# Kernel tuning notes

Measured on AMD Instinct MI355X. Metric: run time of the kernel, lower is better.

## Reference

```python
import jax, jax.numpy as jnp
import numpy as np

DIM = 128
SQRT_DIM = float(np.sqrt(DIM))


def setup_inputs() -> dict:
    key = jax.random.key(0)
    k1, k2, k3, k4 = jax.random.split(key, 4)
    B, S, D = 16, 2048, DIM
    return {
        "query": jax.random.normal(k1, (B, S, D), dtype=jnp.float32),
        "key": jax.random.normal(k2, (B, S, D), dtype=jnp.float32),
        "value": jax.random.normal(k3, (B, S, D), dtype=jnp.float32),
        "trust_score": jax.random.uniform(k4, (B, 1, S), dtype=jnp.float32, minval=0.05, maxval=1.0),
    }


def reference(query, key, value, trust_score):
    # score: [B, q, k]
    score = jnp.einsum("bqd,bkd->bqk", query, key) / SQRT_DIM
    score = score * trust_score
    attn = jax.nn.softmax(score, axis=-1)
    # trust reweighting + renormalization
    attn = attn * trust_score
    attn = attn / jnp.sum(attn, axis=-1, keepdims=True)
    context = jnp.einsum("bqk,bkd->bqd", attn, value)
    return context
```

## Files before the change

kernel.cpp:

```cpp
#include <hip/hip_runtime.h>
#include <math.h>

#define SEQ 2048
#define DIM 128
#define KVB 32
#define NTILES (SEQ / KVB)
#define NT2 (NTILES / 2)
#define KTB 8192
#define VTB 8192

typedef __attribute__((ext_vector_type(8))) short bf16x8;
typedef __attribute__((ext_vector_type(16))) float f32x16;
typedef __attribute__((ext_vector_type(4))) short short4v;
typedef __attribute__((ext_vector_type(4))) float f32x4;

union frag_u { bf16x8 h; unsigned u[4]; };

__device__ __forceinline__ short f2bf(float f) {
  union { float f; unsigned u; } v; v.f = f;
  unsigned r = v.u + 0x7FFFu + ((v.u >> 16) & 1u);
  return (short)(r >> 16);
}
__device__ __forceinline__ float bf2f(short h) {
  return __uint_as_float(((unsigned)(unsigned short)h) << 16);
}
__device__ __forceinline__ void dma16(const void* g, void* l) {
  __builtin_amdgcn_global_load_lds(
      (const __attribute__((address_space(1))) void*)g,
      (__attribute__((address_space(3))) void*)l, 16, 0, 0);
}
__device__ __forceinline__ unsigned cvtpk(float lo, float hi) {
  unsigned r;
  asm("v_cvt_pk_bf16_f32 %0, %1, %2" : "=v"(r) : "v"(lo), "v"(hi));
  return r;
}
__device__ __forceinline__ void pl32swap(unsigned& a, unsigned& b) {
  asm("v_permlane32_swap_b32 %0, %1" : "+v"(a), "+v"(b));
}

__global__ __launch_bounds__(256)
void prepack_kernel(const float* __restrict__ Kg, const float* __restrict__ Vg,
                    const float* __restrict__ Tg,
                    char* __restrict__ Kws, char* __restrict__ Vws,
                    unsigned* __restrict__ Lws) {
  const int tile = blockIdx.x, b = blockIdx.y;
  const int tid = (int)threadIdx.x;
  const float* Kb = Kg + ((size_t)b * SEQ + tile * KVB) * DIM;
  const float* Vb = Vg + ((size_t)b * SEQ + tile * KVB) * DIM;
  const float* Tb = Tg + (size_t)b * SEQ + tile * KVB;
  char* kd = Kws + (size_t)(b * NTILES + tile) * KTB;
  char* vd = Vws + (size_t)(b * NTILES + tile) * VTB;

  #pragma unroll
  for (int i = 0; i < 2; ++i) {
    int id = i * 256 + tid;
    int k = id >> 4, c16 = id & 15;
    float sc = Tb[k] * 0.12751743f;
    const float4 f0 = *(const float4*)(Kb + (size_t)k * DIM + c16 * 8);
    const float4 f1 = *(const float4*)(Kb + (size_t)k * DIM + c16 * 8 + 4);
    bf16x8 pk;
    pk[0]=f2bf(f0.x*sc); pk[1]=f2bf(f0.y*sc); pk[2]=f2bf(f0.z*sc); pk[3]=f2bf(f0.w*sc);
    pk[4]=f2bf(f1.x*sc); pk[5]=f2bf(f1.y*sc); pk[6]=f2bf(f1.z*sc); pk[7]=f2bf(f1.w*sc);
    *(bf16x8*)(kd + k * 256 + ((c16 ^ (k & 7)) << 4)) = pk;
  }
  #pragma unroll
  for (int i = 0; i < 2; ++i) {
    int id = i * 256 + tid;
    int d = id & 127, ch = id >> 7;
    const float* src = Vb + (size_t)(ch * 8) * DIM + d;
    bf16x8 pk;
    #pragma unroll
    for (int j = 0; j < 8; ++j) pk[j] = f2bf(src[(size_t)j * DIM]);
    *(bf16x8*)(vd + d * 64 + ((ch ^ ((d >> 1) & 3)) << 4)) = pk;
  }
  if (tid < KVB) {
    float t = Tb[tid];
    float lt = log2f(t);
    short h = f2bf(lt);
    short lo = f2bf(lt - bf2f(h));
    Lws[(size_t)b * SEQ + tile * KVB + tid] =
        (unsigned)(unsigned short)h | ((unsigned)(unsigned short)lo << 16);
  }
}

__global__ __launch_bounds__(256, 2)
void trust_attn_main(const float* __restrict__ Qg, const char* __restrict__ Kws,
                     const char* __restrict__ Vws, const unsigned* __restrict__ Lws,
                     float* __restrict__ Og, int swz) {
  __shared__ __align__(16) char smem[65536];

  const int bid = (int)blockIdx.x;
  int b, qblk;
  if (swz) { int xcd = bid & 7, idx = bid >> 3; b = xcd * 2 + (idx >> 5); qblk = idx & 31; }
  else     { b = bid >> 5; qblk = bid & 31; }

  const int tid = (int)threadIdx.x;
  const int h   = tid >> 7;
  const int gq  = (tid >> 6) & 1;
  const int l   = tid & 63;
  const int hi  = l >> 5, l31 = l & 31;
  const int t128 = tid & 127;
  const int qcol = qblk * 64 + gq * 32 + l31;

  const float* Qr = Qg + ((size_t)b * SEQ + qcol) * DIM;
  const char* Kt = Kws + (size_t)(b * NTILES + h * NT2) * KTB;
  const char* Vt = Vws + (size_t)(b * NTILES + h * NT2) * VTB;
  const unsigned* Lb = Lws + (size_t)b * SEQ + h * (NT2 * KVB);

  frag_u qf[8];
  #pragma unroll
  for (int c = 0; c < 8; ++c) {
    const float4 a = *(const float4*)(Qr + c * 16 + hi * 8);
    const float4 d = *(const float4*)(Qr + c * 16 + hi * 8 + 4);
    bf16x8 q8;
    q8[0]=f2bf(a.x); q8[1]=f2bf(a.y); q8[2]=f2bf(a.z); q8[3]=f2bf(a.w);
    q8[4]=f2bf(d.x); q8[5]=f2bf(d.y); q8[6]=f2bf(d.z); q8[7]=f2bf(d.w);
    qf[c].h = q8;
  }
  frag_u qpad;
  qpad.u[0] = (hi == 0) ? 0x3F803F80u : 0u;
  qpad.u[1] = qpad.u[2] = qpad.u[3] = 0u;

  f32x16 acc[4];
  #pragma unroll
  for (int nt = 0; nt < 4; ++nt)
    #pragma unroll
    for (int i = 0; i < 16; ++i) acc[nt][i] = 0.f;
  float lsum = 0.f;

  auto ISSUE = [&](int t, int buf) {
    const char* ks = Kt + (size_t)t * KTB;
    const char* vs = Vt + (size_t)t * VTB;
    char* kl = smem + (h * 2 + buf) * 8192;
    char* vl = smem + 32768 + (h * 2 + buf) * 8192;
    #pragma unroll
    for (int j = 0; j < 2; ++j) {
      dma16(ks + j * 4096 + t128 * 16, kl + j * 4096 + t128 * 16);
      dma16(ks + j * 4096 + 2048 + t128 * 16, kl + j * 4096 + 2048 + t128 * 16);
      dma16(vs + j * 4096 + t128 * 16, vl + j * 4096 + t128 * 16);
      dma16(vs + j * 4096 + 2048 + t128 * 16, vl + j * 4096 + 2048 + t128 * 16);
    }
  };

  ISSUE(0, 0);
  unsigned ltc = Lb[l31];
  __syncthreads();

  for (int t = 0; t < NT2; ++t) {
    const int cur = t & 1;
    unsigned ltn = 0;
    if (t + 1 < NT2) {
      ISSUE(t + 1, cur ^ 1);
      ltn = Lb[(t + 1) * KVB + l31];
    }

    const char* Kc = smem + (h * 2 + cur) * 8192;
    const char* Vc = smem + 32768 + (h * 2 + cur) * 8192;

    f32x16 S;
    #pragma unroll
    for (int i = 0; i < 16; ++i) S[i] = 0.f;
    #pragma unroll
    for (int c = 0; c < 8; ++c) {
      frag_u kf;
      kf.h = *(const bf16x8*)(Kc + l31 * 256 + (((2 * c + hi) ^ (l31 & 7)) << 4));
      S = __builtin_amdgcn_mfma_f32_32x32x16_bf16(kf.h, qf[c].h, S, 0, 0, 0);
    }
    frag_u pa;
    pa.u[0] = (hi == 0) ? ltc : 0u;
    pa.u[1] = pa.u[2] = pa.u[3] = 0u;
    S = __builtin_amdgcn_mfma_f32_32x32x16_bf16(pa.h, qpad.h, S, 0, 0, 0);

    float p[16];
    #pragma unroll
    for (int i = 0; i < 16; ++i) {
      p[i] = __builtin_amdgcn_exp2f(S[i]);
      lsum += p[i];
    }

    frag_u PA[2];
    #pragma unroll
    for (int ks = 0; ks < 2; ++ks) {
      unsigned a0 = cvtpk(p[8*ks+0], p[8*ks+1]);
      unsigned a1 = cvtpk(p[8*ks+2], p[8*ks+3]);
      unsigned b0 = cvtpk(p[8*ks+4], p[8*ks+5]);
      unsigned b1 = cvtpk(p[8*ks+6], p[8*ks+7]);
      pl32swap(a0, b0);
      pl32swap(a1, b1);
      PA[ks].u[0] = a0; PA[ks].u[1] = a1; PA[ks].u[2] = b0; PA[ks].u[3] = b1;
    }

    #pragma unroll
    for (int nt = 0; nt < 4; ++nt)
      #pragma unroll
      for (int ks = 0; ks < 2; ++ks) {
        frag_u vf;
        vf.h = *(const bf16x8*)(Vc + (nt * 32 + l31) * 64 + (((2 * ks + hi) ^ ((l31 >> 1) & 3)) << 4));
        acc[nt] = __builtin_amdgcn_mfma_f32_32x32x16_bf16(vf.h, PA[ks].h, acc[nt], 0, 0, 0);
      }

    ltc = ltn;
    __syncthreads();
  }

  const float Z = lsum + __shfl_xor(lsum, 32);
  float* AccX = (float*)smem;
  float* Zx   = (float*)(smem + 32768);
  const int q2 = gq * 32 + l31;

  if (h == 1) {
    if (hi == 0) Zx[q2] = Z;
    #pragma unroll
    for (int nt = 0; nt < 4; ++nt)
      #pragma unroll
      for (int j = 0; j < 4; ++j) {
        int d = nt * 32 + j * 8 + hi * 4;
        int byte_off = (q2 * 512 + d * 4) ^ ((l31 & 7) << 4);
        f32x4 qd;
        qd[0] = acc[nt][j*4+0]; qd[1] = acc[nt][j*4+1];
        qd[2] = acc[nt][j*4+2]; qd[3] = acc[nt][j*4+3];
        *(f32x4*)((char*)AccX + byte_off) = qd;
      }
  }
  __syncthreads();
  if (h == 0) {
    const float inv = 1.0f / (Z + Zx[q2]);
    float* orow = Og + ((size_t)b * SEQ + qcol) * DIM;
    #pragma unroll
    for (int nt = 0; nt < 4; ++nt)
      #pragma unroll
      for (int j = 0; j < 4; ++j) {
        int d = nt * 32 + j * 8 + hi * 4;
        int byte_off = (q2 * 512 + d * 4) ^ ((l31 & 7) << 4);
        f32x4 o = *(const f32x4*)((const char*)AccX + byte_off);
        float4 r;
        r.x = (acc[nt][j*4+0] + o[0]) * inv;
        r.y = (acc[nt][j*4+1] + o[1]) * inv;
        r.z = (acc[nt][j*4+2] + o[2]) * inv;
        r.w = (acc[nt][j*4+3] + o[3]) * inv;
        *(float4*)(orow + d) = r;
      }
  }
}

__global__ __launch_bounds__(256, 2)
void trust_attn_fallback(const float* __restrict__ Qg, const float* __restrict__ Kg,
                         const float* __restrict__ Vg, const float* __restrict__ Tg,
                         float* __restrict__ Og) {
  __shared__ short Klds[2][64 * DIM];
  __shared__ short Vlds[2][DIM * 64];
  __shared__ short Plds[4][16 * 64];
  __shared__ float Tlds[2][64];

  const int b = blockIdx.y;
  const int qbase = blockIdx.x * 64;
  const int tid = (int)threadIdx.x;
  const int w = tid >> 6;
  const int l = tid & 63;
  const int lr = l & 15;
  const int lg = l >> 4;

  const float* Qb = Qg + (size_t)b * SEQ * DIM;
  const float* Kb = Kg + (size_t)b * SEQ * DIM;
  const float* Vb = Vg + (size_t)b * SEQ * DIM;
  const float* Tb = Tg + (size_t)b * SEQ;
  float*       Ob = Og + (size_t)b * SEQ * DIM;

  float4 kreg[8];
  float  vreg[32];
  float  treg;

  auto ISSUE = [&](int kv0) {
    #pragma unroll
    for (int i = 0; i < 8; ++i) {
      int flat4 = i * 256 + tid;
      int r = flat4 >> 5;
      int c4 = (flat4 & 31) << 2;
      kreg[i] = *(const float4*)(Kb + (size_t)(kv0 + r) * DIM + c4);
    }
    #pragma unroll
    for (int i = 0; i < 4; ++i) {
      int task = i * 256 + tid;
      int d = task & 127;
      int chunk = task >> 7;
      const float* src = Vb + (size_t)(kv0 + chunk * 8) * DIM + d;
      #pragma unroll
      for (int j = 0; j < 8; ++j) vreg[i * 8 + j] = src[(size_t)j * DIM];
    }
    treg = (tid < 64) ? Tb[kv0 + tid] : 0.f;
  };

  auto STORE = [&](int buf) {
    #pragma unroll
    for (int i = 0; i < 8; ++i) {
      int flat4 = i * 256 + tid;
      int r = flat4 >> 5;
      int c4 = (flat4 & 31) << 2;
      short4v pk;
      pk[0] = f2bf(kreg[i].x); pk[1] = f2bf(kreg[i].y);
      pk[2] = f2bf(kreg[i].z); pk[3] = f2bf(kreg[i].w);
      int byte_off = (r * 256 + (c4 << 1)) ^ ((r & 7) << 4);
      *(short4v*)((char*)&Klds[buf][0] + byte_off) = pk;
    }
    #pragma unroll
    for (int i = 0; i < 4; ++i) {
      int task = i * 256 + tid;
      int d = task & 127;
      int chunk = task >> 7;
      bf16x8 pk;
      #pragma unroll
      for (int j = 0; j < 8; ++j) pk[j] = f2bf(vreg[i * 8 + j]);
      int byte_off = (d * 128 + chunk * 16) ^ ((d & 7) << 4);
      *(bf16x8*)((char*)&Vlds[buf][0] + byte_off) = pk;
    }
    if (tid < 64) Tlds[buf][tid] = treg;
  };

  bf16x8 qf[4];
  {
    const float* qrow = Qb + (size_t)(qbase + w * 16 + lr) * DIM;
    #pragma unroll
    for (int kk = 0; kk < 4; ++kk) {
      const float4 a = *(const float4*)(qrow + kk * 32 + lg * 8);
      const float4 c = *(const float4*)(qrow + kk * 32 + lg * 8 + 4);
      bf16x8 f;
      f[0] = f2bf(a.x); f[1] = f2bf(a.y); f[2] = f2bf(a.z); f[3] = f2bf(a.w);
      f[4] = f2bf(c.x); f[5] = f2bf(c.y); f[6] = f2bf(c.z); f[7] = f2bf(c.w);
      qf[kk] = f;
    }
  }

  f32x4 acc[8];
  #pragma unroll
  for (int nt = 0; nt < 8; ++nt) acc[nt] = f32x4{0.f, 0.f, 0.f, 0.f};
  float lsum[4] = {0.f, 0.f, 0.f, 0.f};

  ISSUE(0);
  STORE(0);
  __syncthreads();

  for (int t = 0; t < SEQ / 64; ++t) {
    const int cur = t & 1;
    if (t + 1 < SEQ / 64) ISSUE((t + 1) * 64);

    const short* Kc = &Klds[cur][0];
    const short* Vc = &Vlds[cur][0];

    f32x4 s[4];
    #pragma unroll
    for (int kt = 0; kt < 4; ++kt) {
      f32x4 a0 = f32x4{0.f, 0.f, 0.f, 0.f};
      #pragma unroll
      for (int kk = 0; kk < 4; ++kk) {
        int row = kt * 16 + lr;
        int byte_off = (row * 256 + ((kk * 32 + lg * 8) << 1)) ^ ((row & 7) << 4);
        bf16x8 kf = *(const bf16x8*)((const char*)Kc + byte_off);
        a0 = __builtin_amdgcn_mfma_f32_16x16x32_bf16(qf[kk], kf, a0, 0, 0, 0);
      }
      s[kt] = a0;
    }

    short* Pw = Plds[w];
    #pragma unroll
    for (int kt = 0; kt < 4; ++kt) {
      float tt = Tlds[cur][kt * 16 + lr];
      float tc = tt * 0.12751743f;
      #pragma unroll
      for (int r = 0; r < 4; ++r) {
        float p = tt * exp2f(s[kt][r] * tc);
        lsum[r] += p;
        int q = lg * 4 + r;
        int byte_off = ((q * 128) + ((kt * 16 + lr) << 1)) ^ ((q & 7) << 4);
        *(short*)((char*)Pw + byte_off) = f2bf(p);
      }
    }
    asm volatile("s_waitcnt lgkmcnt(0)" ::: "memory");

    #pragma unroll
    for (int ks = 0; ks < 2; ++ks) {
      int byteA = (lr * 128 + ((ks * 32 + lg * 8) << 1)) ^ ((lr & 7) << 4);
      bf16x8 pf = *(const bf16x8*)((char*)Pw + byteA);
      #pragma unroll
      for (int nt = 0; nt < 8; ++nt) {
        int row = nt * 16 + lr;
        int byteB = (row * 128 + ((ks * 32 + lg * 8) << 1)) ^ ((row & 7) << 4);
        bf16x8 vf = *(const bf16x8*)((const char*)Vc + byteB);
        acc[nt] = __builtin_amdgcn_mfma_f32_16x16x32_bf16(pf, vf, acc[nt], 0, 0, 0);
      }
    }

    if (t + 1 < SEQ / 64) {
      STORE(cur ^ 1);
      __syncthreads();
    }
  }

  #pragma unroll
  for (int r = 0; r < 4; ++r) {
    float v = lsum[r];
    v += __shfl_xor(v, 1);
    v += __shfl_xor(v, 2);
    v += __shfl_xor(v, 4);
    v += __shfl_xor(v, 8);
    float inv = 1.0f / v;
    float* dst = Ob + (size_t)(qbase + w * 16 + lg * 4 + r) * DIM + lr;
    #pragma unroll
    for (int nt = 0; nt < 8; ++nt)
      dst[nt * 16] = acc[nt][r] * inv;
  }
}

extern "C" void kernel_launch(void* const* d_in, const int* in_sizes, int n_in,
                              void* d_out, int out_size, void* d_ws, size_t ws_size,
                              hipStream_t stream) {
  (void)n_in; (void)out_size;
  const float* Q = (const float*)d_in[0];
  const float* K = (const float*)d_in[1];
  const float* V = (const float*)d_in[2];
  const float* T = (const float*)d_in[3];
  float* O = (float*)d_out;
  const int B = in_sizes[0] / (SEQ * DIM);

  const size_t kv_bytes = (size_t)B * NTILES * KTB;
  const size_t need = kv_bytes * 2 + (size_t)B * SEQ * sizeof(unsigned);
  if (ws_size >= need) {
    char* Kws = (char*)d_ws;
    char* Vws = Kws + kv_bytes;
    unsigned* Lws = (unsigned*)(Vws + kv_bytes);
    dim3 gridp(NTILES, B);
    prepack_kernel<<<gridp, 256, 0, stream>>>(K, V, T, Kws, Vws, Lws);
    const int nblk = B * (SEQ / 64);
    const int swz = (B == 16) ? 1 : 0;
    trust_attn_main<<<nblk, 256, 0, stream>>>(Q, Kws, Vws, Lws, O, swz);
  } else {
    dim3 grid(SEQ / 64, B);
    trust_attn_fallback<<<grid, 256, 0, stream>>>(Q, K, V, T, O);
  }
}
```

Measured before the change: 65.24 us.

## Drop LDS double buffering to raise occupancy, add MFMA priority hints

Shrinks shared memory from 64KB to 32KB by replacing the double-buffered K/V staging with a single buffer loaded synchronously each iteration, and raises launch bounds to allow more resident blocks per CU. The idea is to hide memory latency through more concurrent workgroups rather than intra-block prefetch. It also wraps the MFMA sections in s_setprio to favour matrix issue across waves. The Z exchange is moved to separate syncs because the smem region it used no longer exists. The risk is exposed load latency per tile and register pressure under the tighter launch bound, which could cause spills.

```diff
diff --git a/kernel.cpp b/kernel.cpp
--- a/kernel.cpp
+++ b/kernel.cpp
@@ -83,11 +83,11 @@
   }
 }
 
-__global__ __launch_bounds__(256, 2)
+__global__ __launch_bounds__(256, 5)
 void trust_attn_main(const float* __restrict__ Qg, const char* __restrict__ Kws,
                      const char* __restrict__ Vws, const unsigned* __restrict__ Lws,
                      float* __restrict__ Og, int swz) {
-  __shared__ __align__(16) char smem[65536];
+  __shared__ __align__(16) char smem[32768];
 
   const int bid = (int)blockIdx.x;
   int b, qblk;
@@ -107,6 +107,9 @@
   const char* Vt = Vws + (size_t)(b * NTILES + h * NT2) * VTB;
   const unsigned* Lb = Lws + (size_t)b * SEQ + h * (NT2 * KVB);
 
+  char* const Kc = smem + h * 8192;
+  char* const Vc = smem + 16384 + h * 8192;
+
   frag_u qf[8];
   #pragma unroll
   for (int c = 0; c < 8; ++c) {
@@ -128,38 +131,27 @@
     for (int i = 0; i < 16; ++i) acc[nt][i] = 0.f;
   float lsum = 0.f;
 
-  auto ISSUE = [&](int t, int buf) {
+  auto ISSUE = [&](int t) {
     const char* ks = Kt + (size_t)t * KTB;
     const char* vs = Vt + (size_t)t * VTB;
-    char* kl = smem + (h * 2 + buf) * 8192;
-    char* vl = smem + 32768 + (h * 2 + buf) * 8192;
     #pragma unroll
     for (int j = 0; j < 2; ++j) {
-      dma16(ks + j * 4096 + t128 * 16, kl + j * 4096 + t128 * 16);
-      dma16(ks + j * 4096 + 2048 + t128 * 16, kl + j * 4096 + 2048 + t128 * 16);
-      dma16(vs + j * 4096 + t128 * 16, vl + j * 4096 + t128 * 16);
-      dma16(vs + j * 4096 + 2048 + t128 * 16, vl + j * 4096 + 2048 + t128 * 16);
+      dma16(ks + j * 4096 + t128 * 16, Kc + j * 4096 + t128 * 16);
+      dma16(ks + j * 4096 + 2048 + t128 * 16, Kc + j * 4096 + 2048 + t128 * 16);
+      dma16(vs + j * 4096 + t128 * 16, Vc + j * 4096 + t128 * 16);
+      dma16(vs + j * 4096 + 2048 + t128 * 16, Vc + j * 4096 + 2048 + t128 * 16);
     }
   };
 
-  ISSUE(0, 0);
-  unsigned ltc = Lb[l31];
-  __syncthreads();
-
   for (int t = 0; t < NT2; ++t) {
-    const int cur = t & 1;
-    unsigned ltn = 0;
-    if (t + 1 < NT2) {
-      ISSUE(t + 1, cur ^ 1);
-      ltn = Lb[(t + 1) * KVB + l31];
-    }
-
-    const char* Kc = smem + (h * 2 + cur) * 8192;
-    const char* Vc = smem + 32768 + (h * 2 + cur) * 8192;
+    const unsigned ltc = Lb[t * KVB + l31];
+    ISSUE(t);
+    __syncthreads();
 
     f32x16 S;
     #pragma unroll
     for (int i = 0; i < 16; ++i) S[i] = 0.f;
+    __builtin_amdgcn_s_setprio(1);
     #pragma unroll
     for (int c = 0; c < 8; ++c) {
       frag_u kf;
@@ -170,6 +162,7 @@
     pa.u[0] = (hi == 0) ? ltc : 0u;
     pa.u[1] = pa.u[2] = pa.u[3] = 0u;
     S = __builtin_amdgcn_mfma_f32_32x32x16_bf16(pa.h, qpad.h, S, 0, 0, 0);
+    __builtin_amdgcn_s_setprio(0);
 
     float p[16];
     #pragma unroll
@@ -190,6 +183,7 @@
       PA[ks].u[0] = a0; PA[ks].u[1] = a1; PA[ks].u[2] = b0; PA[ks].u[3] = b1;
     }
 
+    __builtin_amdgcn_s_setprio(1);
     #pragma unroll
     for (int nt = 0; nt < 4; ++nt)
       #pragma unroll
@@ -198,18 +192,23 @@
         vf.h = *(const bf16x8*)(Vc + (nt * 32 + l31) * 64 + (((2 * ks + hi) ^ ((l31 >> 1) & 3)) << 4));
         acc[nt] = __builtin_amdgcn_mfma_f32_32x32x16_bf16(vf.h, PA[ks].h, acc[nt], 0, 0, 0);
       }
-
-    ltc = ltn;
+    __builtin_amdgcn_s_setprio(0);
+
     __syncthreads();
   }
 
   const float Z = lsum + __shfl_xor(lsum, 32);
+  const int q2 = gq * 32 + l31;
+  float* Zx = (float*)(smem + 16384);
+
+  if (h == 1 && hi == 0) Zx[q2] = Z;
+  __syncthreads();
+  float zoth = 0.f;
+  if (h == 0) zoth = Zx[q2];
+  __syncthreads();
+
   float* AccX = (float*)smem;
-  float* Zx   = (float*)(smem + 32768);
-  const int q2 = gq * 32 + l31;
-
   if (h == 1) {
-    if (hi == 0) Zx[q2] = Z;
     #pragma unroll
     for (int nt = 0; nt < 4; ++nt)
       #pragma unroll
@@ -224,7 +223,7 @@
   }
   __syncthreads();
   if (h == 0) {
-    const float inv = 1.0f / (Z + Zx[q2]);
+    const float inv = 1.0f / (Z + zoth);
     float* orow = Og + ((size_t)b * SEQ + qcol) * DIM;
     #pragma unroll
     for (int nt = 0; nt < 4; ++nt)
```

Measured after the change: 145.4 us. +122.8%, slower.

## Software-pipeline PV MFMAs of previous tile with QK MFMAs of current tile

Applied to the files above, without the earlier changes.

Restructures the attention main loop so the P·V MFMAs for tile t-1 are interleaved with the Q·K MFMAs for tile t, using P fragments and V fragments held in registers across iterations, with a prologue and an epilogue. The goal is to hide the exp/pack dependency latency between QK and PV and keep the matrix units busy. It also adds s_setprio around the MFMA bursts. The cost is higher register pressure from keeping 8 V fragments and the packed P across iterations, which could lower occupancy.

```diff
diff --git a/kernel.cpp b/kernel.cpp
--- a/kernel.cpp
+++ b/kernel.cpp
@@ -128,6 +128,9 @@
     for (int i = 0; i < 16; ++i) acc[nt][i] = 0.f;
   float lsum = 0.f;
 
+  frag_u PAp[2];
+  frag_u vfr[8];
+
   auto ISSUE = [&](int t, int buf) {
     const char* ks = Kt + (size_t)t * KTB;
     const char* vs = Vt + (size_t)t * VTB;
@@ -142,43 +145,13 @@
     }
   };
 
-  ISSUE(0, 0);
-  unsigned ltc = Lb[l31];
-  __syncthreads();
-
-  for (int t = 0; t < NT2; ++t) {
-    const int cur = t & 1;
-    unsigned ltn = 0;
-    if (t + 1 < NT2) {
-      ISSUE(t + 1, cur ^ 1);
-      ltn = Lb[(t + 1) * KVB + l31];
-    }
-
-    const char* Kc = smem + (h * 2 + cur) * 8192;
-    const char* Vc = smem + 32768 + (h * 2 + cur) * 8192;
-
-    f32x16 S;
-    #pragma unroll
-    for (int i = 0; i < 16; ++i) S[i] = 0.f;
-    #pragma unroll
-    for (int c = 0; c < 8; ++c) {
-      frag_u kf;
-      kf.h = *(const bf16x8*)(Kc + l31 * 256 + (((2 * c + hi) ^ (l31 & 7)) << 4));
-      S = __builtin_amdgcn_mfma_f32_32x32x16_bf16(kf.h, qf[c].h, S, 0, 0, 0);
-    }
-    frag_u pa;
-    pa.u[0] = (hi == 0) ? ltc : 0u;
-    pa.u[1] = pa.u[2] = pa.u[3] = 0u;
-    S = __builtin_amdgcn_mfma_f32_32x32x16_bf16(pa.h, qpad.h, S, 0, 0, 0);
-
+  auto EXPPACK = [&](f32x16& S) {
     float p[16];
     #pragma unroll
     for (int i = 0; i < 16; ++i) {
       p[i] = __builtin_amdgcn_exp2f(S[i]);
       lsum += p[i];
     }
-
-    frag_u PA[2];
     #pragma unroll
     for (int ks = 0; ks < 2; ++ks) {
       unsigned a0 = cvtpk(p[8*ks+0], p[8*ks+1]);
@@ -187,21 +160,91 @@
       unsigned b1 = cvtpk(p[8*ks+6], p[8*ks+7]);
       pl32swap(a0, b0);
       pl32swap(a1, b1);
-      PA[ks].u[0] = a0; PA[ks].u[1] = a1; PA[ks].u[2] = b0; PA[ks].u[3] = b1;
-    }
-
-    #pragma unroll
-    for (int nt = 0; nt < 4; ++nt)
-      #pragma unroll
-      for (int ks = 0; ks < 2; ++ks) {
-        frag_u vf;
-        vf.h = *(const bf16x8*)(Vc + (nt * 32 + l31) * 64 + (((2 * ks + hi) ^ ((l31 >> 1) & 3)) << 4));
-        acc[nt] = __builtin_amdgcn_mfma_f32_32x32x16_bf16(vf.h, PA[ks].h, acc[nt], 0, 0, 0);
-      }
-
+      PAp[ks].u[0] = a0; PAp[ks].u[1] = a1; PAp[ks].u[2] = b0; PAp[ks].u[3] = b1;
+    }
+  };
+
+  auto LOADV = [&](const char* Vc) {
+    #pragma unroll
+    for (int g = 0; g < 8; ++g) {
+      int nt = g >> 1, ks = g & 1;
+      vfr[g].h = *(const bf16x8*)(Vc + (nt * 32 + l31) * 64 +
+                  (((2 * ks + hi) ^ ((l31 >> 1) & 3)) << 4));
+    }
+  };
+
+  ISSUE(0, 0);
+  unsigned ltc = Lb[l31];
+  __syncthreads();
+
+  {
+    const char* Kc = smem;
+    const char* Vc = smem + 32768;
+    const char* Kch = Kc + (h * 2) * 8192;
+    const char* Vch = Vc + (h * 2) * 8192;
+    ISSUE(1, 1);
+    unsigned ltn = Lb[KVB + l31];
+
+    f32x16 S;
+    #pragma unroll
+    for (int i = 0; i < 16; ++i) S[i] = 0.f;
+    __builtin_amdgcn_s_setprio(1);
+    #pragma unroll
+    for (int c = 0; c < 8; ++c) {
+      frag_u kfc;
+      kfc.h = *(const bf16x8*)(Kch + l31 * 256 + (((2 * c + hi) ^ (l31 & 7)) << 4));
+      S = __builtin_amdgcn_mfma_f32_32x32x16_bf16(kfc.h, qf[c].h, S, 0, 0, 0);
+    }
+    frag_u pa;
+    pa.u[0] = (hi == 0) ? ltc : 0u;
+    pa.u[1] = pa.u[2] = pa.u[3] = 0u;
+    S = __builtin_amdgcn_mfma_f32_32x32x16_bf16(pa.h, qpad.h, S, 0, 0, 0);
+    __builtin_amdgcn_s_setprio(0);
+
+    EXPPACK(S);
+    LOADV(Vch);
     ltc = ltn;
     __syncthreads();
   }
+
+  for (int t = 1; t < NT2; ++t) {
+    const int cur = t & 1;
+    unsigned ltn = 0;
+    if (t + 1 < NT2) {
+      ISSUE(t + 1, cur ^ 1);
+      ltn = Lb[(t + 1) * KVB + l31];
+    }
+    const char* Kc = smem + (h * 2 + cur) * 8192;
+    const char* Vc = smem + 32768 + (h * 2 + cur) * 8192;
+
+    f32x16 S;
+    #pragma unroll
+    for (int i = 0; i < 16; ++i) S[i] = 0.f;
+    __builtin_amdgcn_s_setprio(1);
+    #pragma unroll
+    for (int c = 0; c < 8; ++c) {
+      frag_u kfc;
+      kfc.h = *(const bf16x8*)(Kc + l31 * 256 + (((2 * c + hi) ^ (l31 & 7)) << 4));
+      S = __builtin_amdgcn_mfma_f32_32x32x16_bf16(kfc.h, qf[c].h, S, 0, 0, 0);
+      acc[c >> 1] = __builtin_amdgcn_mfma_f32_32x32x16_bf16(vfr[c].h, PAp[c & 1].h, acc[c >> 1], 0, 0, 0);
+    }
+    frag_u pa;
+    pa.u[0] = (hi == 0) ? ltc : 0u;
+    pa.u[1] = pa.u[2] = pa.u[3] = 0u;
+    S = __builtin_amdgcn_mfma_f32_32x32x16_bf16(pa.h, qpad.h, S, 0, 0, 0);
+    __builtin_amdgcn_s_setprio(0);
+
+    EXPPACK(S);
+    LOADV(Vc);
+    ltc = ltn;
+    __syncthreads();
+  }
+
+  __builtin_amdgcn_s_setprio(1);
+  #pragma unroll
+  for (int c = 0; c < 8; ++c)
+    acc[c >> 1] = __builtin_amdgcn_mfma_f32_32x32x16_bf16(vfr[c].h, PAp[c & 1].h, acc[c >> 1], 0, 0, 0);
+  __builtin_amdgcn_s_setprio(0);
 
   const float Z = lsum + __shfl_xor(lsum, 32);
   float* AccX = (float*)smem;
```

Result: faster. 62.24 us, median of 2 (-4.6%).
